# Optimization experiments

Measured on AMD Instinct MI355X. Metric: run time of the kernel, lower is better.

Reference implementation:

```python
import jax, jax.numpy as jnp
import numpy as np

N, E, D, ED, L = 40000, 640000, 128, 16, 3  # nodes, edges, emb_dim, edge_dim, num_layer
BN_EPS = 1e-5


def setup_inputs() -> dict:
    key = jax.random.key(0)
    ks = jax.random.split(key, 20)
    s = 0.05
    inp = {
        "x": jax.random.normal(ks[0], (N, D), jnp.float32),
        "edge_attr": jax.random.normal(ks[1], (E, ED), jnp.float32),
        # node encoder Linear(input_dim, emb_dim)
        "node_W": jax.random.normal(ks[2], (D, D), jnp.float32) * s,
        "node_b": jnp.zeros((D,), jnp.float32),
        # per-layer params (leading dim L)
        "edge_W": jax.random.normal(ks[3], (L, ED, D), jnp.float32) * s,
        "edge_b": jnp.zeros((L, D), jnp.float32),
        "attn_W": jax.random.normal(ks[4], (L, 2 * D, 1), jnp.float32) * s,
        "attn_b": jnp.zeros((L, 1), jnp.float32),
        "eps": jnp.zeros((L,), jnp.float32),
        "W1": jax.random.normal(ks[5], (L, D, 2 * D), jnp.float32) * s,
        "b1": jnp.zeros((L, 2 * D), jnp.float32),
        "bn1_g": jnp.ones((L, 2 * D), jnp.float32),
        "bn1_b": jnp.zeros((L, 2 * D), jnp.float32),
        "W2": jax.random.normal(ks[6], (L, 2 * D, D), jnp.float32) * s,
        "b2": jnp.zeros((L, D), jnp.float32),
        "bn_g": jnp.ones((L, D), jnp.float32),
        "bn_b": jnp.zeros((L, D), jnp.float32),
        "edge_index": jax.random.randint(ks[7], (2, E), 0, N, jnp.int32),
    }
    return inp


def _bn_eval(h, g, b):
    # BatchNorm1d in eval with running_mean=0, running_var=1
    return g * h * (1.0 / np.sqrt(1.0 + BN_EPS)) + b


def reference(x, edge_attr, node_W, node_b, edge_W, edge_b, attn_W, attn_b,
              eps, W1, b1, bn1_g, bn1_b, W2, b2, bn_g, bn_b, edge_index):
    src, dst = edge_index[0], edge_index[1]
    h = x @ node_W + node_b  # node_encoder, [N, D]
    for l in range(L):
        e = edge_attr @ edge_W[l] + edge_b[l]       # [E, D] edge embedding
        xj = h[src]                                  # [E, D] source gather
        xi = h[dst]                                  # [E, D] target gather
        a = jax.nn.sigmoid(jnp.concatenate([xi, xj], axis=-1) @ attn_W[l] + attn_b[l])  # [E,1]
        msg = jax.nn.relu(xj * a + e)                # fused per-edge message
        agg = jax.ops.segment_sum(msg, dst, num_segments=N)  # scatter-add aggregate
        z = (1.0 + eps[l]) * h + agg
        # GIN mlp: Linear -> BN(eval) -> ReLU -> Linear
        z = _bn_eval(z @ W1[l] + b1[l], bn1_g[l], bn1_b[l])
        z = jax.nn.relu(z)
        z = z @ W2[l] + b2[l]
        # outer BatchNorm(eval); dropout = identity in eval; JK='last', no residual
        z = _bn_eval(z, bn_g[l], bn_b[l])
        if l < L - 1:
            z = jax.nn.relu(z)
        h = z
    return h
```

## Files before the change

### kernel.cpp

```cpp
#include <hip/hip_runtime.h>
#include <math.h>

#define NN 40000
#define EE 640000
#define DD 128
#define EDD 16
#define LL 3
#define TEB 128

__device__ __constant__ float kBnInv = 0.9999950000374997f;

typedef __bf16 bf16x8 __attribute__((ext_vector_type(8)));
typedef float  f32x4  __attribute__((ext_vector_type(4)));
typedef float  f32x2  __attribute__((ext_vector_type(2)));

__device__ __forceinline__ unsigned pack_bf2(float a, float b) {
    unsigned ua = __float_as_uint(a), ub = __float_as_uint(b);
    ua = (ua + 0x7fffu + ((ua >> 16) & 1u)) >> 16;
    ub = (ub + 0x7fffu + ((ub >> 16) & 1u)) & 0xffff0000u;
    return ua | ub;
}
__device__ __forceinline__ unsigned short bf16r(float x) {
    unsigned u = __float_as_uint(x);
    u = (u + 0x7fffu + ((u >> 16) & 1u)) >> 16;
    return (unsigned short)u;
}

__global__ __launch_bounds__(256) void node_enc_kernel(
    const float* __restrict__ x, const float* __restrict__ W,
    const float* __restrict__ b,
    const float* __restrict__ aW, const float* __restrict__ eps_p,
    float* __restrict__ h, unsigned* __restrict__ hb,
    float* __restrict__ pi, float* __restrict__ pj, float* __restrict__ z)
{
    __shared__ float xs[32][DD];
    const int t = threadIdx.x;
    const long rowbase = (long)blockIdx.x * 32;

    const float4* x4 = (const float4*)(x + rowbase * DD);
    float4* xs4 = (float4*)&xs[0][0];
#pragma unroll
    for (int i = 0; i < 4; i++) xs4[t + i * 256] = x4[t + i * 256];
    __syncthreads();

    const int c  = (t & 31) * 4;
    const int r0 = (t >> 5) * 4;

    float acc[4][4] = {};
    for (int k4 = 0; k4 < DD; k4 += 4) {
        float4 xr[4];
#pragma unroll
        for (int i = 0; i < 4; i++) xr[i] = *(const float4*)&xs[r0 + i][k4];
#pragma unroll
        for (int kk = 0; kk < 4; kk++) {
            const float4 w = *(const float4*)(W + (k4 + kk) * DD + c);
#pragma unroll
            for (int i = 0; i < 4; i++) {
                const float xv = ((const float*)&xr[i])[kk];
                acc[i][0] = fmaf(xv, w.x, acc[i][0]);
                acc[i][1] = fmaf(xv, w.y, acc[i][1]);
                acc[i][2] = fmaf(xv, w.z, acc[i][2]);
                acc[i][3] = fmaf(xv, w.w, acc[i][3]);
            }
        }
    }
    const float4 bv  = *(const float4*)(b + c);
    const float4 awi = *(const float4*)(aW + c);
    const float4 awj = *(const float4*)(aW + DD + c);
    const float ep = 1.0f + eps_p[0];

    float pa[4], pb[4];
#pragma unroll
    for (int i = 0; i < 4; i++) {
        const long row = rowbase + r0 + i;
        float4 ov = { acc[i][0] + bv.x, acc[i][1] + bv.y,
                      acc[i][2] + bv.z, acc[i][3] + bv.w };
        *(float4*)(h + row * DD + c) = ov;
        uint2 pv = { pack_bf2(ov.x, ov.y), pack_bf2(ov.z, ov.w) };
        *(uint2*)(hb + row * 64 + (c >> 1)) = pv;
        float4 zv = { ep * ov.x, ep * ov.y, ep * ov.z, ep * ov.w };
        *(float4*)(z + row * DD + c) = zv;
        pa[i] = ov.x * awi.x + ov.y * awi.y + ov.z * awi.z + ov.w * awi.w;
        pb[i] = ov.x * awj.x + ov.y * awj.y + ov.z * awj.z + ov.w * awj.w;
    }
#pragma unroll
    for (int off = 1; off < 32; off <<= 1) {
#pragma unroll
        for (int i = 0; i < 4; i++) {
            pa[i] += __shfl_xor(pa[i], off, 64);
            pb[i] += __shfl_xor(pb[i], off, 64);
        }
    }
    if ((t & 31) == 0) {
#pragma unroll
        for (int i = 0; i < 4; i++) {
            pi[rowbase + r0 + i] = pa[i];
            pj[rowbase + r0 + i] = pb[i];
        }
    }
}

__global__ __launch_bounds__(256) void wcast_kernel(
    const float* __restrict__ W1, const float* __restrict__ W2,
    unsigned short* __restrict__ w1t, unsigned short* __restrict__ w2t)
{
    const int idx = blockIdx.x * 256 + threadIdx.x;
    const int l = idx >> 15, r = idx & 32767;
    {   const int n = r >> 7, k = r & 127;
        w1t[idx] = bf16r(W1[(l << 15) + (k << 8) + n]);
    }
    {   const int n = r >> 8, k = r & 255;
        w2t[idx] = bf16r(W2[(l << 15) + (k << 7) + n]);
    }
}

__global__ __launch_bounds__(256) void hist_kernel(
    const int* __restrict__ edge_index, int* __restrict__ counts)
{
    const int i = blockIdx.x * 256 + threadIdx.x;
    atomicAdd(&counts[edge_index[EE + i]], 1);
}

__global__ __launch_bounds__(256) void scan1_kernel(
    const int* __restrict__ counts, int* __restrict__ scanned,
    int* __restrict__ partials)
{
    __shared__ int sdata[256];
    const int t = threadIdx.x;
    const int base = blockIdx.x * 1024 + t * 4;
    int v[4]; int sum = 0;
#pragma unroll
    for (int i = 0; i < 4; i++) {
        const int idx = base + i;
        v[i] = (idx < NN) ? counts[idx] : 0;
        sum += v[i];
    }
    sdata[t] = sum;
    __syncthreads();
    for (int off = 1; off < 256; off <<= 1) {
        int x = (t >= off) ? sdata[t - off] : 0;
        __syncthreads();
        sdata[t] += x;
        __syncthreads();
    }
    int run = sdata[t] - sum;
#pragma unroll
    for (int i = 0; i < 4; i++) {
        const int idx = base + i;
        if (idx < NN) scanned[idx] = run;
        run += v[i];
    }
    if (t == 255) partials[blockIdx.x] = sdata[255];
}

__global__ void scan2_kernel(int* __restrict__ partials)
{
    if (threadIdx.x == 0) {
        int run = 0;
        for (int i = 0; i < 40; i++) { int v = partials[i]; partials[i] = run; run += v; }
    }
}

__global__ __launch_bounds__(256) void scan3_kernel(
    const int* __restrict__ scanned, const int* __restrict__ partials,
    int* __restrict__ offsets, int* __restrict__ cursor)
{
    const int idx = blockIdx.x * 256 + threadIdx.x;
    if (idx < NN) {
        const int off = scanned[idx] + partials[idx >> 10];
        offsets[idx] = off;
        cursor[idx]  = off;
    }
}

__global__ __launch_bounds__(256) void scatter_kernel(
    const int* __restrict__ edge_index, const float* __restrict__ edge_attr,
    int* __restrict__ cursor,
    int* __restrict__ srcs_p, int* __restrict__ dstd_p,
    unsigned* __restrict__ ea_b)
{
    const int i = blockIdx.x * 256 + threadIdx.x;
    const int src = edge_index[i];
    const int dst = edge_index[EE + i];
    const int pos = atomicAdd(&cursor[dst], 1);
    srcs_p[pos] = src << 6;
    dstd_p[pos] = dst << 7;

    const float4* sp = (const float4*)(edge_attr + (long)i * EDD);
    const float4 s0 = sp[0], s1 = sp[1], s2 = sp[2], s3 = sp[3];
    uint4 o0 = { pack_bf2(s0.x, s0.y), pack_bf2(s0.z, s0.w),
                 pack_bf2(s1.x, s1.y), pack_bf2(s1.z, s1.w) };
    uint4 o1 = { pack_bf2(s2.x, s2.y), pack_bf2(s2.z, s2.w),
                 pack_bf2(s3.x, s3.y), pack_bf2(s3.z, s3.w) };
    *(uint4*)(ea_b + (long)pos * 8)     = o0;
    *(uint4*)(ea_b + (long)pos * 8 + 4) = o1;
}

__global__ __launch_bounds__(256) void edge_msg_kernel(
    const unsigned* __restrict__ hb, const unsigned* __restrict__ ea_b,
    const float* __restrict__ pi, const float* __restrict__ pj,
    const int* __restrict__ srcs_p, const int* __restrict__ dstd_p,
    const float* __restrict__ ab_p,
    const float* __restrict__ eW, const float* __restrict__ eb,
    float* __restrict__ z)
{
    __shared__ unsigned sh_hb[TEB * 64];
    __shared__ unsigned sh_ea[TEB * 8];
    __shared__ int      sh_src[TEB];
    __shared__ int      sh_dst[TEB];
    __shared__ float    sh_a[TEB];

    const int t = threadIdx.x;
    const long e0 = (long)blockIdx.x * TEB;

    if (t < TEB) {
        const int ss = srcs_p[e0 + t];
        const int dd = dstd_p[e0 + t];
        sh_src[t] = ss;
        sh_dst[t] = dd;
        const float s = pi[dd >> 7] + pj[ss >> 6] + ab_p[0];
        sh_a[t] = 1.0f / (1.0f + expf(-s));
    }
    __syncthreads();

    {
        const int chunk = t & 15;
        const int r0    = t >> 4;
#pragma unroll
        for (int i = 0; i < TEB / 16; i++) {
            const int row  = r0 + 16 * i;
            const int srow = sh_src[row];
            *(uint4*)&sh_hb[row * 64 + chunk * 4] =
                *(const uint4*)(hb + srow + chunk * 4);
        }
        ((uint4*)sh_ea)[t] = ((const uint4*)(ea_b + e0 * 8))[t];
    }
    __syncthreads();

    const int wid = t >> 6, lane = t & 63;
    const int c0 = lane * 2;
    const int base = wid * (TEB / 4);

    f32x2 ew[EDD];
#pragma unroll
    for (int q = 0; q < EDD; q++) {
        const float2 w2 = ((const float2*)(eW + q * DD))[lane];
        ew[q][0] = w2.x; ew[q][1] = w2.y;
    }
    const float2 ebf = ((const float2*)eb)[lane];
    const f32x2 ebv = { ebf.x, ebf.y };
    const f32x2 zero2 = { 0.0f, 0.0f };

    f32x2 acc = zero2;
    int cur = sh_dst[base];

#pragma unroll 4
    for (int j = 0; j < TEB / 4; j++) {
        const int   dd = sh_dst[base + j];
        const float a  = sh_a[base + j];
        const unsigned u = sh_hb[(base + j) * 64 + lane];

        const uint4 ua = *(const uint4*)&sh_ea[(base + j) * 8];
        const uint4 ub = *(const uint4*)&sh_ea[(base + j) * 8 + 4];
        const unsigned es[8] = { ua.x, ua.y, ua.z, ua.w,
                                 ub.x, ub.y, ub.z, ub.w };
        f32x2 ev = ebv;
#pragma unroll
        for (int q = 0; q < 8; q++) {
            const float f0 = __uint_as_float(es[q] << 16);
            const float f1 = __uint_as_float(es[q] & 0xffff0000u);
            const f32x2 v0 = { f0, f0 }, v1 = { f1, f1 };
            ev = __builtin_elementwise_fma(v0, ew[2 * q],     ev);
            ev = __builtin_elementwise_fma(v1, ew[2 * q + 1], ev);
        }

        if (dd != cur) {
            atomicAdd(&z[cur + c0],     acc[0]);
            atomicAdd(&z[cur + c0 + 1], acc[1]);
            acc = zero2; cur = dd;
        }
        const f32x2 xj = { __uint_as_float(u << 16),
                           __uint_as_float(u & 0xffff0000u) };
        const f32x2 av = { a, a };
        f32x2 m = __builtin_elementwise_fma(xj, av, ev);
        m = __builtin_elementwise_max(m, zero2);
        acc += m;
    }
    atomicAdd(&z[cur + c0],     acc[0]);
    atomicAdd(&z[cur + c0 + 1], acc[1]);
}

__global__ __launch_bounds__(256) void mlp_mfma_kernel(
    const float* __restrict__ zin,
    const unsigned short* __restrict__ w1t, const unsigned short* __restrict__ w2t,
    const float* __restrict__ b1, const float* __restrict__ g1, const float* __restrict__ bb1,
    const float* __restrict__ b2, const float* __restrict__ g2, const float* __restrict__ bb2,
    const float* __restrict__ aWn, const float* __restrict__ epsn_p,
    float* __restrict__ out, unsigned* __restrict__ hb,
    float* __restrict__ pi, float* __restrict__ pj, float* __restrict__ z,
    const int do_relu)
{
    __shared__ __align__(16) unsigned short zsb[64][136];
    __shared__ __align__(16) unsigned short usb[64][264];
    const int t = threadIdx.x;
    const int wid = t >> 6, lane = t & 63;
    const long rowbase = (long)blockIdx.x * 64;

    {
        const float4* z4 = (const float4*)(zin + rowbase * DD);
#pragma unroll
        for (int i = 0; i < 8; i++) {
            const int idx = t + i * 256;
            const float4 v = z4[idx];
            const int row = idx >> 5;
            const int c4  = (idx & 31) * 4;
            uint2 pv = { pack_bf2(v.x, v.y), pack_bf2(v.z, v.w) };
            *(uint2*)&zsb[row][c4] = pv;
        }
    }
    __syncthreads();

    const int mrow  = lane & 15;
    const int quad  = lane >> 4;
    const int mbase = wid * 16;
    const f32x4 vzero = {0.0f, 0.0f, 0.0f, 0.0f};

    bf16x8 af[4];
#pragma unroll
    for (int ks = 0; ks < 4; ks++)
        af[ks] = *(const bf16x8*)&zsb[mbase + mrow][ks * 32 + quad * 8];

    f32x4 acc[16];
#pragma unroll
    for (int i = 0; i < 16; i++) acc[i] = vzero;

#pragma unroll
    for (int nt = 0; nt < 16; nt++) {
        const unsigned short* wp = w1t + (nt * 16 + mrow) * 128 + quad * 8;
#pragma unroll
        for (int ks = 0; ks < 4; ks++) {
            const bf16x8 bfr = *(const bf16x8*)(wp + ks * 32);
            acc[nt] = __builtin_amdgcn_mfma_f32_16x16x32_bf16(af[ks], bfr, acc[nt], 0, 0, 0);
        }
    }

#pragma unroll
    for (int nt = 0; nt < 16; nt++) {
        const int c = nt * 16 + mrow;
        const float g = g1[c], bi = b1[c], bt = bb1[c];
#pragma unroll
        for (int r = 0; r < 4; r++) {
            const int row = mbase + quad * 4 + r;
            const float u = fmaxf(fmaf(g * (acc[nt][r] + bi), kBnInv, bt), 0.0f);
            const float up = __shfl_xor(u, 1, 64);
            if ((mrow & 1) == 0)
                *(unsigned*)&usb[row][c] = pack_bf2(u, up);
        }
    }
    __syncthreads();

    bf16x8 af2[8];
#pragma unroll
    for (int ks = 0; ks < 8; ks++)
        af2[ks] = *(const bf16x8*)&usb[mbase + mrow][ks * 32 + quad * 8];

    f32x4 acc2[8];
#pragma unroll
    for (int i = 0; i < 8; i++) acc2[i] = vzero;

#pragma unroll
    for (int nt = 0; nt < 8; nt++) {
        const unsigned short* wp = w2t + (nt * 16 + mrow) * 256 + quad * 8;
#pragma unroll
        for (int ks = 0; ks < 8; ks++) {
            const bf16x8 bfr = *(const bf16x8*)(wp + ks * 32);
            acc2[nt] = __builtin_amdgcn_mfma_f32_16x16x32_bf16(af2[ks], bfr, acc2[nt], 0, 0, 0);
        }
    }

    float awn_i[8], awn_j[8];
    float epn = 0.0f;
    if (do_relu) {
#pragma unroll
        for (int nt = 0; nt < 8; nt++) {
            awn_i[nt] = aWn[nt * 16 + mrow];
            awn_j[nt] = aWn[DD + nt * 16 + mrow];
        }
        epn = 1.0f + epsn_p[0];
    }
    float si[4] = {0, 0, 0, 0}, sj[4] = {0, 0, 0, 0};

#pragma unroll
    for (int nt = 0; nt < 8; nt++) {
        const int c = nt * 16 + mrow;
        const float g = g2[c], bi = b2[c], bt = bb2[c];
#pragma unroll
        for (int r = 0; r < 4; r++) {
            const long row = rowbase + mbase + quad * 4 + r;
            float v = fmaf(g * (acc2[nt][r] + bi), kBnInv, bt);
            if (do_relu) {
                v = fmaxf(v, 0.0f);
                z[row * DD + c] = epn * v;
                si[r] = fmaf(v, awn_i[nt], si[r]);
                sj[r] = fmaf(v, awn_j[nt], sj[r]);
            }
            out[row * DD + c] = v;
            const float vp = __shfl_xor(v, 1, 64);
            if ((mrow & 1) == 0)
                hb[row * 64 + (c >> 1)] = pack_bf2(v, vp);
        }
    }
    if (do_relu) {
#pragma unroll
        for (int off = 1; off < 16; off <<= 1) {
#pragma unroll
            for (int r = 0; r < 4; r++) {
                si[r] += __shfl_xor(si[r], off, 64);
                sj[r] += __shfl_xor(sj[r], off, 64);
            }
        }
        if (mrow == 0) {
#pragma unroll
            for (int r = 0; r < 4; r++) {
                const long row = rowbase + mbase + quad * 4 + r;
                pi[row] = si[r];
                pj[row] = sj[r];
            }
        }
    }
}

extern "C" void kernel_launch(void* const* d_in, const int* in_sizes, int n_in,
                              void* d_out, int out_size, void* d_ws, size_t ws_size,
                              hipStream_t stream)
{
    const float* x         = (const float*)d_in[0];
    const float* edge_attr = (const float*)d_in[1];
    const float* node_W    = (const float*)d_in[2];
    const float* node_b    = (const float*)d_in[3];
    const float* edge_W    = (const float*)d_in[4];
    const float* edge_b    = (const float*)d_in[5];
    const float* attn_W    = (const float*)d_in[6];
    const float* attn_b    = (const float*)d_in[7];
    const float* eps       = (const float*)d_in[8];
    const float* W1        = (const float*)d_in[9];
    const float* b1        = (const float*)d_in[10];
    const float* bn1_g     = (const float*)d_in[11];
    const float* bn1_b     = (const float*)d_in[12];
    const float* W2        = (const float*)d_in[13];
    const float* b2        = (const float*)d_in[14];
    const float* bn_g      = (const float*)d_in[15];
    const float* bn_b      = (const float*)d_in[16];
    const int*   edge_index= (const int*)d_in[17];

    float* h    = (float*)d_ws;
    float* z    = h + (size_t)NN * DD;
    float* pi   = z + (size_t)NN * DD;
    float* pj   = pi + NN;
    unsigned* ea_b = (unsigned*)(pj + NN);
    unsigned* hbuf = ea_b + (size_t)EE * 8;
    unsigned short* w1t = (unsigned short*)(hbuf + (size_t)NN * 64);
    unsigned short* w2t = w1t + (size_t)LL * 32768;
    int* counts  = (int*)(w2t + (size_t)LL * 32768);
    int* offsets = counts + NN;
    int* cursor  = offsets + NN;
    int* scanned = cursor + NN;
    int* partials= scanned + 40960;
    int* srcs_p  = partials + 64;
    int* dstd_p  = srcs_p + EE;
    float* out = (float*)d_out;

    node_enc_kernel<<<NN / 32, 256, 0, stream>>>(
        x, node_W, node_b, attn_W, eps, h, hbuf, pi, pj, z);
    wcast_kernel<<<LL * 128, 256, 0, stream>>>(W1, W2, w1t, w2t);

    hipMemsetAsync(counts, 0, NN * sizeof(int), stream);
    hist_kernel<<<EE / 256, 256, 0, stream>>>(edge_index, counts);
    scan1_kernel<<<40, 256, 0, stream>>>(counts, scanned, partials);
    scan2_kernel<<<1, 64, 0, stream>>>(partials);
    scan3_kernel<<<(NN + 255) / 256, 256, 0, stream>>>(scanned, partials, offsets, cursor);
    scatter_kernel<<<EE / 256, 256, 0, stream>>>(
        edge_index, edge_attr, cursor, srcs_p, dstd_p, ea_b);

    for (int l = 0; l < LL; l++) {
        const int ln = (l + 1 < LL) ? (l + 1) : l;
        edge_msg_kernel<<<EE / TEB, 256, 0, stream>>>(
            hbuf, ea_b, pi, pj, srcs_p, dstd_p, attn_b + l,
            edge_W + (size_t)l * EDD * DD, edge_b + (size_t)l * DD, z);
        mlp_mfma_kernel<<<NN / 64, 256, 0, stream>>>(
            z,
            w1t + (size_t)l * 32768, w2t + (size_t)l * 32768,
            b1 + (size_t)l * 2 * DD, bn1_g + (size_t)l * 2 * DD, bn1_b + (size_t)l * 2 * DD,
            b2 + (size_t)l * DD, bn_g + (size_t)l * DD, bn_b + (size_t)l * DD,
            attn_W + (size_t)ln * 2 * DD, eps + ln,
            (l == LL - 1) ? out : h, hbuf, pi, pj, z, (l < LL - 1) ? 1 : 0);
    }
}
```

Measured before the change: 588.7 us.

## Split MLP GEMM columns across waves; shrink edge tile and pre-decode edge attrs

The MLP kernel now gives each wave a fixed slice of output columns. Its W1/W2 fragments are held in registers while it loops over the four 16-row tiles, so each wave no longer streams the full weight matrices from global memory. Attention dot products are combined with shared-memory atomics before being written to pi/pj. The edge-message kernel halves its edge tile to 64 and decodes bf16 edge attributes to fp32 once in shared memory, so the inner loop drops the per-edge unpacking. This costs more shared traffic for edge attributes, and the smaller edge tile means more blocks and more boundary atomics.

```diff
diff --git a/kernel.cpp b/kernel.cpp
--- a/kernel.cpp
+++ b/kernel.cpp
@@ -6,7 +6,7 @@
 #define DD 128
 #define EDD 16
 #define LL 3
-#define TEB 128
+#define TEB 64
 
 __device__ __constant__ float kBnInv = 0.9999950000374997f;
 
@@ -205,7 +205,7 @@
     float* __restrict__ z)
 {
     __shared__ unsigned sh_hb[TEB * 64];
-    __shared__ unsigned sh_ea[TEB * 8];
+    __shared__ float    sh_ea[TEB * EDD];
     __shared__ int      sh_src[TEB];
     __shared__ int      sh_dst[TEB];
     __shared__ float    sh_a[TEB];
@@ -233,7 +233,15 @@
             *(uint4*)&sh_hb[row * 64 + chunk * 4] =
                 *(const uint4*)(hb + srow + chunk * 4);
         }
-        ((uint4*)sh_ea)[t] = ((const uint4*)(ea_b + e0 * 8))[t];
+#pragma unroll
+        for (int i = 0; i < 2; i++) {
+            const int idx  = t * 2 + i;
+            const int edge = idx >> 3, q = idx & 7;
+            const unsigned u = ea_b[e0 * 8 + idx];
+            float2 f = { __uint_as_float(u << 16),
+                         __uint_as_float(u & 0xffff0000u) };
+            *(float2*)&sh_ea[edge * EDD + q * 2] = f;
+        }
     }
     __syncthreads();
 
@@ -260,18 +268,15 @@
         const float a  = sh_a[base + j];
         const unsigned u = sh_hb[(base + j) * 64 + lane];
 
-        const uint4 ua = *(const uint4*)&sh_ea[(base + j) * 8];
-        const uint4 ub = *(const uint4*)&sh_ea[(base + j) * 8 + 4];
-        const unsigned es[8] = { ua.x, ua.y, ua.z, ua.w,
-                                 ub.x, ub.y, ub.z, ub.w };
+        const float4* eap = (const float4*)&sh_ea[(base + j) * EDD];
+        const float4 t0 = eap[0], t1 = eap[1], t2 = eap[2], t3 = eap[3];
+        const float ea[EDD] = { t0.x,t0.y,t0.z,t0.w, t1.x,t1.y,t1.z,t1.w,
+                                t2.x,t2.y,t2.z,t2.w, t3.x,t3.y,t3.z,t3.w };
         f32x2 ev = ebv;
 #pragma unroll
-        for (int q = 0; q < 8; q++) {
-            const float f0 = __uint_as_float(es[q] << 16);
-            const float f1 = __uint_as_float(es[q] & 0xffff0000u);
-            const f32x2 v0 = { f0, f0 }, v1 = { f1, f1 };
-            ev = __builtin_elementwise_fma(v0, ew[2 * q],     ev);
-            ev = __builtin_elementwise_fma(v1, ew[2 * q + 1], ev);
+        for (int q = 0; q < EDD; q++) {
+            const f32x2 eaq = { ea[q], ea[q] };
+            ev = __builtin_elementwise_fma(eaq, ew[q], ev);
         }
 
         if (dd != cur) {
@@ -302,9 +307,12 @@
 {
     __shared__ __align__(16) unsigned short zsb[64][136];
     __shared__ __align__(16) unsigned short usb[64][264];
+    __shared__ float sh_pi[64], sh_pj[64];
     const int t = threadIdx.x;
     const int wid = t >> 6, lane = t & 63;
     const long rowbase = (long)blockIdx.x * 64;
+
+    if (t < 64) { sh_pi[t] = 0.0f; sh_pj[t] = 0.0f; }
 
     {
         const float4* z4 = (const float4*)(zin + rowbase * DD);
@@ -322,110 +330,131 @@
 
     const int mrow  = lane & 15;
     const int quad  = lane >> 4;
-    const int mbase = wid * 16;
     const f32x4 vzero = {0.0f, 0.0f, 0.0f, 0.0f};
 
-    bf16x8 af[4];
-#pragma unroll
-    for (int ks = 0; ks < 4; ks++)
-        af[ks] = *(const bf16x8*)&zsb[mbase + mrow][ks * 32 + quad * 8];
-
-    f32x4 acc[16];
-#pragma unroll
-    for (int i = 0; i < 16; i++) acc[i] = vzero;
-
-#pragma unroll
-    for (int nt = 0; nt < 16; nt++) {
-        const unsigned short* wp = w1t + (nt * 16 + mrow) * 128 + quad * 8;
-#pragma unroll
-        for (int ks = 0; ks < 4; ks++) {
-            const bf16x8 bfr = *(const bf16x8*)(wp + ks * 32);
-            acc[nt] = __builtin_amdgcn_mfma_f32_16x16x32_bf16(af[ks], bfr, acc[nt], 0, 0, 0);
-        }
-    }
-
-#pragma unroll
-    for (int nt = 0; nt < 16; nt++) {
-        const int c = nt * 16 + mrow;
-        const float g = g1[c], bi = b1[c], bt = bb1[c];
-#pragma unroll
-        for (int r = 0; r < 4; r++) {
-            const int row = mbase + quad * 4 + r;
-            const float u = fmaxf(fmaf(g * (acc[nt][r] + bi), kBnInv, bt), 0.0f);
-            const float up = __shfl_xor(u, 1, 64);
-            if ((mrow & 1) == 0)
-                *(unsigned*)&usb[row][c] = pack_bf2(u, up);
+    {
+        const int nt0 = wid * 4;
+        bf16x8 bf[4][4];
+#pragma unroll
+        for (int j = 0; j < 4; j++) {
+            const unsigned short* wp = w1t + ((nt0 + j) * 16 + mrow) * 128 + quad * 8;
+#pragma unroll
+            for (int ks = 0; ks < 4; ks++)
+                bf[j][ks] = *(const bf16x8*)(wp + ks * 32);
+        }
+        float gg[4], bi[4], bt[4];
+#pragma unroll
+        for (int j = 0; j < 4; j++) {
+            const int c = (nt0 + j) * 16 + mrow;
+            gg[j] = g1[c]; bi[j] = b1[c]; bt[j] = bb1[c];
+        }
+#pragma unroll
+        for (int rt = 0; rt < 4; rt++) {
+            bf16x8 af[4];
+#pragma unroll
+            for (int ks = 0; ks < 4; ks++)
+                af[ks] = *(const bf16x8*)&zsb[rt * 16 + mrow][ks * 32 + quad * 8];
+            f32x4 acc[4];
+#pragma unroll
+            for (int j = 0; j < 4; j++) acc[j] = vzero;
+#pragma unroll
+            for (int j = 0; j < 4; j++)
+#pragma unroll
+                for (int ks = 0; ks < 4; ks++)
+                    acc[j] = __builtin_amdgcn_mfma_f32_16x16x32_bf16(af[ks], bf[j][ks], acc[j], 0, 0, 0);
+#pragma unroll
+            for (int j = 0; j < 4; j++) {
+                const int c = (nt0 + j) * 16 + mrow;
+#pragma unroll
+                for (int r = 0; r < 4; r++) {
+                    const int row = rt * 16 + quad * 4 + r;
+                    const float u = fmaxf(fmaf(gg[j] * (acc[j][r] + bi[j]), kBnInv, bt[j]), 0.0f);
+                    const float up = __shfl_xor(u, 1, 64);
+                    if ((mrow & 1) == 0)
+                        *(unsigned*)&usb[row][c] = pack_bf2(u, up);
+                }
+            }
         }
     }
     __syncthreads();
 
-    bf16x8 af2[8];
-#pragma unroll
-    for (int ks = 0; ks < 8; ks++)
-        af2[ks] = *(const bf16x8*)&usb[mbase + mrow][ks * 32 + quad * 8];
-
-    f32x4 acc2[8];
-#pragma unroll
-    for (int i = 0; i < 8; i++) acc2[i] = vzero;
-
-#pragma unroll
-    for (int nt = 0; nt < 8; nt++) {
-        const unsigned short* wp = w2t + (nt * 16 + mrow) * 256 + quad * 8;
-#pragma unroll
-        for (int ks = 0; ks < 8; ks++) {
-            const bf16x8 bfr = *(const bf16x8*)(wp + ks * 32);
-            acc2[nt] = __builtin_amdgcn_mfma_f32_16x16x32_bf16(af2[ks], bfr, acc2[nt], 0, 0, 0);
-        }
-    }
-
-    float awn_i[8], awn_j[8];
-    float epn = 0.0f;
+    {
+        const int nt0 = wid * 2;
+        bf16x8 bf[2][8];
+#pragma unroll
+        for (int j = 0; j < 2; j++) {
+            const unsigned short* wp = w2t + ((nt0 + j) * 16 + mrow) * 256 + quad * 8;
+#pragma unroll
+            for (int ks = 0; ks < 8; ks++)
+                bf[j][ks] = *(const bf16x8*)(wp + ks * 32);
+        }
+        float gg[2], bi[2], bt[2], awi[2], awj[2];
+#pragma unroll
+        for (int j = 0; j < 2; j++) {
+            const int c = (nt0 + j) * 16 + mrow;
+            gg[j] = g2[c]; bi[j] = b2[c]; bt[j] = bb2[c];
+            awi[j] = aWn[c]; awj[j] = aWn[DD + c];
+        }
+        const float epn = do_relu ? (1.0f + epsn_p[0]) : 0.0f;
+
+#pragma unroll
+        for (int rt = 0; rt < 4; rt++) {
+            bf16x8 af[8];
+#pragma unroll
+            for (int ks = 0; ks < 8; ks++)
+                af[ks] = *(const bf16x8*)&usb[rt * 16 + mrow][ks * 32 + quad * 8];
+            f32x4 acc[2];
+            acc[0] = vzero; acc[1] = vzero;
+#pragma unroll
+            for (int j = 0; j < 2; j++)
+#pragma unroll
+                for (int ks = 0; ks < 8; ks++)
+                    acc[j] = __builtin_amdgcn_mfma_f32_16x16x32_bf16(af[ks], bf[j][ks], acc[j], 0, 0, 0);
+
+            float si[4] = {0, 0, 0, 0}, sj[4] = {0, 0, 0, 0};
+#pragma unroll
+            for (int j = 0; j < 2; j++) {
+                const int c = (nt0 + j) * 16 + mrow;
+#pragma unroll
+                for (int r = 0; r < 4; r++) {
+                    const long row = rowbase + rt * 16 + quad * 4 + r;
+                    float v = fmaf(gg[j] * (acc[j][r] + bi[j]), kBnInv, bt[j]);
+                    if (do_relu) {
+                        v = fmaxf(v, 0.0f);
+                        z[row * DD + c] = epn * v;
+                        si[r] = fmaf(v, awi[j], si[r]);
+                        sj[r] = fmaf(v, awj[j], sj[r]);
+                    }
+                    out[row * DD + c] = v;
+                    const float vp = __shfl_xor(v, 1, 64);
+                    if ((mrow & 1) == 0)
+                        hb[row * 64 + (c >> 1)] = pack_bf2(v, vp);
+                }
+            }
+            if (do_relu) {
+#pragma unroll
+                for (int off = 1; off < 16; off <<= 1) {
+#pragma unroll
+                    for (int r = 0; r < 4; r++) {
+                        si[r] += __shfl_xor(si[r], off, 64);
+                        sj[r] += __shfl_xor(sj[r], off, 64);
+                    }
+                }
+                if (mrow == 0) {
+#pragma unroll
+                    for (int r = 0; r < 4; r++) {
+                        atomicAdd(&sh_pi[rt * 16 + quad * 4 + r], si[r]);
+                        atomicAdd(&sh_pj[rt * 16 + quad * 4 + r], sj[r]);
+                    }
+                }
+            }
+        }
+    }
     if (do_relu) {
-#pragma unroll
-        for (int nt = 0; nt < 8; nt++) {
-            awn_i[nt] = aWn[nt * 16 + mrow];
-            awn_j[nt] = aWn[DD + nt * 16 + mrow];
-        }
-        epn = 1.0f + epsn_p[0];
-    }
-    float si[4] = {0, 0, 0, 0}, sj[4] = {0, 0, 0, 0};
-
-#pragma unroll
-    for (int nt = 0; nt < 8; nt++) {
-        const int c = nt * 16 + mrow;
-        const float g = g2[c], bi = b2[c], bt = bb2[c];
-#pragma unroll
-        for (int r = 0; r < 4; r++) {
-            const long row = rowbase + mbase + quad * 4 + r;
-            float v = fmaf(g * (acc2[nt][r] + bi), kBnInv, bt);
-            if (do_relu) {
-                v = fmaxf(v, 0.0f);
-                z[row * DD + c] = epn * v;
-                si[r] = fmaf(v, awn_i[nt], si[r]);
-                sj[r] = fmaf(v, awn_j[nt], sj[r]);
-            }
-            out[row * DD + c] = v;
-            const float vp = __shfl_xor(v, 1, 64);
-            if ((mrow & 1) == 0)
-                hb[row * 64 + (c >> 1)] = pack_bf2(v, vp);
-        }
-    }
-    if (do_relu) {
-#pragma unroll
-        for (int off = 1; off < 16; off <<= 1) {
-#pragma unroll
-            for (int r = 0; r < 4; r++) {
-                si[r] += __shfl_xor(si[r], off, 64);
-                sj[r] += __shfl_xor(sj[r], off, 64);
-            }
-        }
-        if (mrow == 0) {
-#pragma unroll
-            for (int r = 0; r < 4; r++) {
-                const long row = rowbase + mbase + quad * 4 + r;
-                pi[row] = si[r];
-                pj[row] = sj[r];
-            }
+        __syncthreads();
+        if (t < 64) {
+            pi[rowbase + t] = sh_pi[t];
+            pj[rowbase + t] = sh_pj[t];
         }
     }
 }
```

Measured after the change: 522.5 us. 1.13x faster.
